# Kernel tuning notes

Measured on AMD Instinct MI355X. Metric: run time of the kernel, lower is better.

Reference implementation:

```python
import jax, jax.numpy as jnp
import numpy as np
import math

D_INNER = 512
D_STATE = 16
DT_RANK = 32
B_SZ = 2
L_SEQ = 4096


def setup_inputs() -> dict:
    key = jax.random.key(0)
    ks = jax.random.split(key, 6)
    x = jax.random.normal(ks[0], (B_SZ, L_SEQ, D_INNER), dtype=jnp.float32)
    # parameters (match torch init semantics closely enough for a numeric baseline)
    A = jnp.arange(1, D_STATE + 1, dtype=jnp.float32)
    A_log = jnp.broadcast_to(jnp.log(A)[None, :], (D_INNER, D_STATE)).copy()
    D_param = jnp.ones((D_INNER,), dtype=jnp.float32)
    # x_proj: Linear(d_inner -> dt_rank + 2*d_state), no bias
    W_xproj = jax.random.normal(ks[1], (DT_RANK + 2 * D_STATE, D_INNER), dtype=jnp.float32) / np.sqrt(D_INNER)
    # dt_proj: Linear(dt_rank -> d_inner) with special bias init
    W_dt = jax.random.normal(ks[2], (D_INNER, DT_RANK), dtype=jnp.float32) / np.sqrt(DT_RANK)
    dt_init = jnp.exp(jax.random.uniform(ks[3], (D_INNER,)) * (math.log(0.1) - math.log(0.001)) + math.log(0.001))
    b_dt = jnp.log(jnp.exp(dt_init) - 1.0)
    alpha = jnp.asarray(0.6, dtype=jnp.float32)
    beta_logit = jnp.asarray(math.log(0.99 / (1.0 - 0.99 + 1e-08)), dtype=jnp.float32)
    return {"x": x, "A_log": A_log, "D_param": D_param, "W_xproj": W_xproj,
            "W_dt": W_dt, "b_dt": b_dt, "alpha": alpha, "beta_logit": beta_logit}


def _momentum_ssm(x, A_log, D_param, W_xproj, W_dt, b_dt, alpha, beta_logit):
    # x: (B, L, D)
    proj = jnp.einsum('bld,pd->blp', x, W_xproj)            # (B, L, r+2N)
    dt_in = proj[..., :DT_RANK]
    Bp = proj[..., DT_RANK:DT_RANK + D_STATE]                # (B, L, N)
    Cp = proj[..., DT_RANK + D_STATE:]                       # (B, L, N)
    dt = jax.nn.softplus(jnp.einsum('blr,dr->bld', dt_in, W_dt) + b_dt)  # (B, L, D)
    A = -jnp.exp(A_log)                                      # (D, N)
    A_bar = jnp.exp(dt[..., None] * A[None, None])           # (B, L, D, N)
    # fused B_bar * x_t: dt * Bp * x
    inp = dt[..., None] * Bp[:, :, None, :] * x[..., None]   # (B, L, D, N)
    beta = jax.nn.sigmoid(beta_logit)

    # scan over time; carry (h, v): (B, D, N)
    h0 = jnp.zeros((x.shape[0], D_INNER, D_STATE), dtype=x.dtype)
    v0 = jnp.zeros_like(h0)

    def step(carry, ts):
        h, v = carry
        a_t, inp_t, c_t = ts                                 # (B,D,N), (B,D,N), (B,N)
        v = beta * v + alpha * inp_t
        h = a_t * h + v
        y = jnp.einsum('bdn,bn->bd', h, c_t)
        return (h, v), y

    xs = (jnp.moveaxis(A_bar, 1, 0), jnp.moveaxis(inp, 1, 0), jnp.moveaxis(Cp, 1, 0))
    _, ys = jax.lax.scan(step, (h0, v0), xs)                 # ys: (L, B, D)
    y = jnp.moveaxis(ys, 0, 1)                               # (B, L, D)
    return y + D_param * x


def reference(x, A_log, D_param, W_xproj, W_dt, b_dt, alpha, beta_logit):
    return _momentum_ssm(x, A_log, D_param, W_xproj, W_dt, b_dt, alpha, beta_logit)
```

## Files before the change

kernel.cpp:

```cpp
#include <hip/hip_runtime.h>


#define D_IN 512
#define D_ST 16
#define DTR  32
#define BSZ  2
#define LSEQ 4096
#define PDIM 64
#define NCH  256
#define LCH  (LSEQ / NCH)
#define LOG2E 1.44269504f
#define LN2   0.69314718f

typedef __attribute__((ext_vector_type(8))) short short8;
typedef __attribute__((ext_vector_type(4))) float f32x4;
typedef _Float16 f16;
typedef __attribute__((ext_vector_type(8))) _Float16 f16x8;

__device__ inline float fast_exp2(float x) { return __builtin_amdgcn_exp2f(x); }
__device__ inline float fast_log2(float x) { return __builtin_amdgcn_logf(x); }

__device__ inline unsigned short bf16_rne(float f) {
  unsigned b = __float_as_uint(f);
  return (unsigned short)((b + 0x7fffu + ((b >> 16) & 1u)) >> 16);
}

__device__ inline void cvt8(const float4 u, const float4 v, short8& hi, short8& lo) {
  float f[8] = {u.x, u.y, u.z, u.w, v.x, v.y, v.z, v.w};
#pragma unroll
  for (int i = 0; i < 8; ++i) {
    unsigned short h = bf16_rne(f[i]);
    hi[i] = (short)h;
    float r = f[i] - __uint_as_float((unsigned)h << 16);
    lo[i] = (short)bf16_rne(r);
  }
}

__device__ inline void st16h(f16* p, const float* s) {
  f16 t[16];
#pragma unroll
  for (int i = 0; i < 16; ++i) t[i] = (f16)s[i];
  *(f16x8*)p = *(f16x8*)&t[0];
  *(f16x8*)(p + 8) = *(f16x8*)&t[8];
}
__device__ inline void ld16h(const f16* p, float* d) {
  f16x8 a = *(const f16x8*)p;
  f16x8 b = *(const f16x8*)(p + 8);
#pragma unroll
  for (int i = 0; i < 8; ++i) { d[i] = (float)a[i]; d[8 + i] = (float)b[i]; }
}

#define PWCHK(val, n)                                                        \
  pw = pw && (fabsf((val) - (float)((n) + 1) * a0) <=                        \
              2e-5f * fabsf((float)((n) + 1) * a0));

__device__ inline bool detectA2(const float* __restrict__ A_log, int d, float& a0) {
  const float4* ap = (const float4*)(A_log + (size_t)d * D_ST);
  float4 r0 = ap[0], r1 = ap[1], r2 = ap[2], r3 = ap[3];
  float4 e0 = make_float4(-__expf(r0.x) * LOG2E, -__expf(r0.y) * LOG2E,
                          -__expf(r0.z) * LOG2E, -__expf(r0.w) * LOG2E);
  float4 e1 = make_float4(-__expf(r1.x) * LOG2E, -__expf(r1.y) * LOG2E,
                          -__expf(r1.z) * LOG2E, -__expf(r1.w) * LOG2E);
  float4 e2 = make_float4(-__expf(r2.x) * LOG2E, -__expf(r2.y) * LOG2E,
                          -__expf(r2.z) * LOG2E, -__expf(r2.w) * LOG2E);
  float4 e3 = make_float4(-__expf(r3.x) * LOG2E, -__expf(r3.y) * LOG2E,
                          -__expf(r3.z) * LOG2E, -__expf(r3.w) * LOG2E);
  a0 = e0.x;
  bool pw = true;
  PWCHK(e0.y, 1) PWCHK(e0.z, 2) PWCHK(e0.w, 3)
  PWCHK(e1.x, 4) PWCHK(e1.y, 5) PWCHK(e1.z, 6) PWCHK(e1.w, 7)
  PWCHK(e2.x, 8) PWCHK(e2.y, 9) PWCHK(e2.z, 10) PWCHK(e2.w, 11)
  PWCHK(e3.x, 12) PWCHK(e3.y, 13) PWCHK(e3.z, 14) PWCHK(e3.w, 15)
  return pw;
}

__global__ __launch_bounds__(256) void k_wprep(const float* __restrict__ W,
                                               short* __restrict__ Whi,
                                               short* __restrict__ Wlo) {
  const int i = (blockIdx.x * 256 + threadIdx.x) * 4;
  float4 w = *(const float4*)(W + i);
  float f[4] = {w.x, w.y, w.z, w.w};
  unsigned short h[4], lo[4];
#pragma unroll
  for (int j = 0; j < 4; ++j) {
    h[j] = bf16_rne(f[j]);
    float r = f[j] - __uint_as_float((unsigned)h[j] << 16);
    lo[j] = bf16_rne(r);
  }
  *(uint2*)(Whi + i) = make_uint2(h[0] | ((unsigned)h[1] << 16), h[2] | ((unsigned)h[3] << 16));
  *(uint2*)(Wlo + i) = make_uint2(lo[0] | ((unsigned)lo[1] << 16), lo[2] | ((unsigned)lo[3] << 16));
}

#define MM3(ACC, AH, AL, BH, BL)                                        \
  ACC = __builtin_amdgcn_mfma_f32_16x16x32_bf16(AL, BH, ACC, 0, 0, 0);  \
  ACC = __builtin_amdgcn_mfma_f32_16x16x32_bf16(AH, BL, ACC, 0, 0, 0);  \
  ACC = __builtin_amdgcn_mfma_f32_16x16x32_bf16(AH, BH, ACC, 0, 0, 0);

#define LOADB(P, S)                                   \
  {                                                   \
    const int kb = ((S) & 15) * 32;                   \
    P##h0 = *(const short8*)(bh + kb);                \
    P##h1 = *(const short8*)(bh + 8192 + kb);         \
    P##h2 = *(const short8*)(bh + 16384 + kb);        \
    P##h3 = *(const short8*)(bh + 24576 + kb);        \
    P##l0 = *(const short8*)(bl + kb);                \
    P##l1 = *(const short8*)(bl + 8192 + kb);         \
    P##l2 = *(const short8*)(bl + 16384 + kb);        \
    P##l3 = *(const short8*)(bl + 24576 + kb);        \
  }

#define LOADA(Aa, Ab, S)                              \
  {                                                   \
    const int ka = ((S) & 15) * 32;                   \
    Aa = *(const float4*)(xr + ka);                   \
    Ab = *(const float4*)(xr + ka + 4);               \
  }

#define SUBSTEP(Aa, Ab, P, SA, SB)                    \
  {                                                   \
    short8 ahi, alo;                                  \
    cvt8(Aa, Ab, ahi, alo);                           \
    MM3(acc0, ahi, alo, P##h0, P##l0);                \
    MM3(acc1, ahi, alo, P##h1, P##l1);                \
    MM3(acc2, ahi, alo, P##h2, P##l2);                \
    MM3(acc3, ahi, alo, P##h3, P##l3);                \
    LOADB(P, SB);                                     \
    LOADA(Aa, Ab, SA);                                \
  }

__global__ __launch_bounds__(64) void k_proj(const float* __restrict__ x,
                                             const short* __restrict__ Whi,
                                             const short* __restrict__ Wlo,
                                             float* __restrict__ proj) {
  const int row0 = blockIdx.x * 16;
  const int l = threadIdx.x;
  const int m = l & 15;
  const int ko = (l >> 4) * 8;
  const float* xr = x + (size_t)(row0 + m) * D_IN + ko;
  const short* bh = Whi + (size_t)m * D_IN + ko;
  const short* bl = Wlo + (size_t)m * D_IN + ko;

  f32x4 acc0 = {0.f, 0.f, 0.f, 0.f}, acc1 = acc0, acc2 = acc0, acc3 = acc0;
  float4 A0a, A0b, A1a, A1b, A2a, A2b, A3a, A3b;
  short8 Xh0, Xh1, Xh2, Xh3, Xl0, Xl1, Xl2, Xl3;
  short8 Yh0, Yh1, Yh2, Yh3, Yl0, Yl1, Yl2, Yl3;
  LOADA(A0a, A0b, 0); LOADA(A1a, A1b, 1); LOADA(A2a, A2b, 2); LOADA(A3a, A3b, 3);
  LOADB(X, 0); LOADB(Y, 1);

#pragma unroll
  for (int it = 0; it < 4; ++it) {
    const int s = it * 4;
    SUBSTEP(A0a, A0b, X, s + 4, s + 2);
    SUBSTEP(A1a, A1b, Y, s + 5, s + 3);
    SUBSTEP(A2a, A2b, X, s + 6, s + 4);
    SUBSTEP(A3a, A3b, Y, s + 7, s + 5);
  }

  const int r0 = (l >> 4) * 4;
#pragma unroll
  for (int r = 0; r < 4; ++r) {
    float* pr = proj + (size_t)(row0 + r0 + r) * PDIM + m;
    pr[0] = acc0[r]; pr[16] = acc1[r]; pr[32] = acc2[r]; pr[48] = acc3[r];
  }
}

#define S1_LOOP                                                              \
  _Pragma("unroll")                                                          \
  for (int j = 0; j < LCH; ++j) {                                            \
    const float4* pj = (const float4*)(pb + j * PDIM);                       \
    float4 pp[8];                                                            \
    _Pragma("unroll")                                                        \
    for (int k = 0; k < 8; ++k) pp[k] = pj[k];                               \
    float c0 = bb, c1 = 0.f, c2 = 0.f, c3 = 0.f;                             \
    _Pragma("unroll")                                                        \
    for (int k = 0; k < 8; ++k) {                                            \
      c0 = fmaf(pp[k].x, w4[k].x, c0);                                       \
      c1 = fmaf(pp[k].y, w4[k].y, c1);                                       \
      c2 = fmaf(pp[k].z, w4[k].z, c2);                                       \
      c3 = fmaf(pp[k].w, w4[k].w, c3);                                       \
    }                                                                        \
    const float acc = (c0 + c1) + (c2 + c3);                                 \
    const float ee = fast_exp2(acc * LOG2E);                                 \
    const float dtc = (acc > 20.f) ? acc : LN2 * fast_log2(1.f + ee);        \
    dp[(size_t)j * D_IN] = (f16)dtc;                                         \
    sd += dtc;                                                               \
    bpow *= beta;                                                            \
    const float u = alpha * dtc * xs[j];                                     \
    float4 bq[4];                                                            \
    _Pragma("unroll")                                                        \
    for (int k = 0; k < 4; ++k) bq[k] = pj[8 + k];                           \
    const float* Bf = (const float*)bq;                                      \
    AR_INIT;                                                                 \
    _Pragma("unroll")                                                        \
    for (int n = 0; n < 16; ++n) {                                           \
      AR_STEP;                                                               \
      v[n] = fmaf(beta, v[n], u * Bf[n]);                                    \
      h[n] = fmaf(ar, h[n], v[n]);                                           \
      cv[n] = fmaf(ar, cv[n], bpow);                                         \
    }                                                                        \
  }

__global__ __launch_bounds__(256) void k_scan1(const float* __restrict__ x,
                                               const float* __restrict__ proj,
                                               const float* __restrict__ A_log,
                                               const float* __restrict__ W_dt,
                                               const float* __restrict__ b_dt,
                                               const float* __restrict__ alpha_p,
                                               const float* __restrict__ beta_p,
                                               f16* __restrict__ hh,
                                               f16* __restrict__ vh,
                                               f16* __restrict__ cvv,
                                               float* __restrict__ sdt,
                                               f16* __restrict__ dth) {
  const int c = blockIdx.x, b = blockIdx.z;
  const int d = blockIdx.y * 256 + threadIdx.x;
  const int t0 = c * LCH;
  const float* pb = proj + ((size_t)b * LSEQ + t0) * PDIM;

  float xs[LCH];
  {
    const float* xp = x + ((size_t)b * LSEQ + t0) * D_IN + d;
#pragma unroll
    for (int j = 0; j < LCH; ++j) xs[j] = xp[(size_t)j * D_IN];
  }
  float4 w4[8];
  {
    const float4* wp = (const float4*)(W_dt + (size_t)d * DTR);
#pragma unroll
    for (int i = 0; i < 8; ++i) w4[i] = wp[i];
  }
  const float bb = b_dt[d];
  const float alpha = alpha_p[0];
  const float beta = 1.f / (1.f + __expf(-beta_p[0]));
  float a0;
  const bool pw = detectA2(A_log, d, a0);

  f16* dp = dth + ((size_t)b * LSEQ + t0) * D_IN + d;
  float h[16] = {}, v[16] = {}, cv[16] = {};
  float bpow = 1.f, sd = 0.f;

  if (pw) {
#define AR_INIT const float r = fast_exp2(dtc * a0); float ar = 1.f
#define AR_STEP ar *= r
    S1_LOOP
#undef AR_INIT
#undef AR_STEP
  } else {
    volatile const float* av = A_log + (size_t)d * D_ST;
#define AR_INIT float ar
#define AR_STEP ar = fast_exp2(dtc * (-__expf(av[n]) * LOG2E))
    S1_LOOP
#undef AR_INIT
#undef AR_STEP
  }

  const size_t base = ((size_t)(b * NCH + c) * D_IN + d) * D_ST;
  st16h(hh + base, h);
  st16h(vh + base, v);
  st16h(cvv + base, cv);
  sdt[(size_t)(b * NCH + c) * D_IN + d] = sd;
}

__global__ __launch_bounds__(64) void k_fix(f16* __restrict__ hh,
                                            f16* __restrict__ vh,
                                            const f16* __restrict__ cvv,
                                            const float* __restrict__ sdt,
                                            const float* __restrict__ A_log,
                                            const float* __restrict__ beta_p) {
  const int g = blockIdx.x * 64 + threadIdx.x;
  const int b = g >> 13;
  const int dn = g & 8191;
  const float beta = 1.f / (1.f + __expf(-beta_p[0]));
  const float A2 = -__expf(A_log[dn]) * LOG2E;
  float bL = beta;
#pragma unroll
  for (int i = 0; i < 4; ++i) bL *= bL;

  const size_t cs = (size_t)D_IN * D_ST;
  const size_t base = (size_t)b * NCH * cs + dn;
  const size_t sbase = (size_t)b * NCH * D_IN + (dn >> 4);

  float hg[8], vg[8], cg[8], sg[8];
#pragma unroll
  for (int i = 0; i < 8; ++i) {
    hg[i] = (float)hh[base + i * cs];
    vg[i] = (float)vh[base + i * cs];
    cg[i] = (float)cvv[base + i * cs];
    sg[i] = sdt[sbase + i * D_IN];
  }
  float H = 0.f, V = 0.f;
  for (int c0 = 0; c0 < NCH; c0 += 8) {
    const int cp = (c0 + 8) & (NCH - 1);
    float hn[8], vn[8], cn[8], sn[8];
#pragma unroll
    for (int i = 0; i < 8; ++i) {
      hn[i] = (float)hh[base + (size_t)(cp + i) * cs];
      vn[i] = (float)vh[base + (size_t)(cp + i) * cs];
      cn[i] = (float)cvv[base + (size_t)(cp + i) * cs];
      sn[i] = sdt[sbase + (size_t)(cp + i) * D_IN];
    }
#pragma unroll
    for (int i = 0; i < 8; ++i) {
      hh[base + (size_t)(c0 + i) * cs] = (f16)H;
      vh[base + (size_t)(c0 + i) * cs] = (f16)V;
      const float Pa = fast_exp2(sg[i] * A2);
      const float Hn = fmaf(Pa, H, fmaf(cg[i], V, hg[i]));
      V = fmaf(bL, V, vg[i]);
      H = Hn;
    }
#pragma unroll
    for (int i = 0; i < 8; ++i) { hg[i] = hn[i]; vg[i] = vn[i]; cg[i] = cn[i]; sg[i] = sn[i]; }
  }
}

#define S2_LOOP                                                              \
  _Pragma("unroll")                                                          \
  for (int j = 0; j < LCH; ++j) {                                            \
    const float4* pj = (const float4*)(pb + j * PDIM);                       \
    float4 bq[8];                                                            \
    _Pragma("unroll")                                                        \
    for (int k = 0; k < 8; ++k) bq[k] = pj[8 + k];                           \
    const float* Bf = (const float*)bq;                                      \
    const float dtc = dtv[j], xv = xs[j];                                    \
    const float u = alpha * dtc * xv;                                        \
    float y0 = 0.f, y1 = 0.f, y2 = 0.f, y3 = 0.f;                            \
    AR_INIT;                                                                 \
    _Pragma("unroll")                                                        \
    for (int n = 0; n < 16; ++n) {                                           \
      AR_STEP;                                                               \
      v[n] = fmaf(beta, v[n], u * Bf[n]);                                    \
      h[n] = fmaf(ar, h[n], v[n]);                                           \
      float hc = h[n] * Bf[16 + n];                                          \
      if ((n & 3) == 0) y0 += hc;                                            \
      else if ((n & 3) == 1) y1 += hc;                                       \
      else if ((n & 3) == 2) y2 += hc;                                       \
      else y3 += hc;                                                         \
    }                                                                        \
    op[(size_t)j * D_IN] = (y0 + y1) + (y2 + y3) + Dv * xv;                  \
  }

__global__ __launch_bounds__(256) void k_scan2(const float* __restrict__ x,
                                               const f16* __restrict__ dth,
                                               const float* __restrict__ proj,
                                               const float* __restrict__ A_log,
                                               const float* __restrict__ D_param,
                                               const float* __restrict__ alpha_p,
                                               const float* __restrict__ beta_p,
                                               const f16* __restrict__ hh,
                                               const f16* __restrict__ vh,
                                               float* __restrict__ out) {
  const int c = blockIdx.x, b = blockIdx.z;
  const int d = blockIdx.y * 256 + threadIdx.x;
  const int t0 = c * LCH;
  const float* pb = proj + ((size_t)b * LSEQ + t0) * PDIM;

  float xs[LCH], dtv[LCH];
  {
    const float* xp = x + ((size_t)b * LSEQ + t0) * D_IN + d;
    const f16* dp = dth + ((size_t)b * LSEQ + t0) * D_IN + d;
#pragma unroll
    for (int j = 0; j < LCH; ++j) xs[j] = xp[(size_t)j * D_IN];
#pragma unroll
    for (int j = 0; j < LCH; ++j) dtv[j] = (float)dp[(size_t)j * D_IN];
  }
  const float alpha = alpha_p[0];
  const float beta = 1.f / (1.f + __expf(-beta_p[0]));
  const float Dv = D_param[d];
  float a0;
  const bool pw = detectA2(A_log, d, a0);
  const size_t ibase = ((size_t)(b * NCH + c) * D_IN + d) * D_ST;
  float h[16], v[16];
  ld16h(hh + ibase, h);
  ld16h(vh + ibase, v);

  float* op = out + ((size_t)b * LSEQ + t0) * D_IN + d;
  if (pw) {
#define AR_INIT const float r = fast_exp2(dtc * a0); float ar = 1.f
#define AR_STEP ar *= r
    S2_LOOP
#undef AR_INIT
#undef AR_STEP
  } else {
    volatile const float* av = A_log + (size_t)d * D_ST;
#define AR_INIT float ar
#define AR_STEP ar = fast_exp2(dtc * (-__expf(av[n]) * LOG2E))
    S2_LOOP
#undef AR_INIT
#undef AR_STEP
  }
}

extern "C" void kernel_launch(void* const* d_in, const int* in_sizes, int n_in,
                              void* d_out, int out_size, void* d_ws, size_t ws_size,
                              hipStream_t stream) {
  const float* x = (const float*)d_in[0];
  const float* A_log = (const float*)d_in[1];
  const float* D_param = (const float*)d_in[2];
  const float* W_xproj = (const float*)d_in[3];
  const float* W_dt = (const float*)d_in[4];
  const float* b_dt = (const float*)d_in[5];
  const float* alpha = (const float*)d_in[6];
  const float* beta_logit = (const float*)d_in[7];
  float* out = (float*)d_out;

  const size_t NST = (size_t)BSZ * NCH * D_IN * D_ST;
  float* ws = (float*)d_ws;
  float* proj = ws;
  float* sdt = proj + (size_t)BSZ * LSEQ * PDIM;
  f16* hh = (f16*)(sdt + (size_t)BSZ * NCH * D_IN);
  f16* vh = hh + NST;
  f16* cvv = vh + NST;
  f16* dth = cvv + NST;
  short* Whi = (short*)(dth + (size_t)BSZ * LSEQ * D_IN);
  short* Wlo = Whi + (size_t)PDIM * D_IN;

  k_wprep<<<dim3(PDIM * D_IN / 1024), dim3(256), 0, stream>>>(W_xproj, Whi, Wlo);
  k_proj<<<dim3(BSZ * LSEQ / 16), dim3(64), 0, stream>>>(x, Whi, Wlo, proj);
  k_scan1<<<dim3(NCH, D_IN / 256, BSZ), dim3(256), 0, stream>>>(
      x, proj, A_log, W_dt, b_dt, alpha, beta_logit, hh, vh, cvv, sdt, dth);
  k_fix<<<dim3(BSZ * D_IN * D_ST / 64), dim3(64), 0, stream>>>(hh, vh, cvv, sdt, A_log,
                                                               beta_logit);
  k_scan2<<<dim3(NCH, D_IN / 256, BSZ), dim3(256), 0, stream>>>(
      x, dth, proj, A_log, D_param, alpha, beta_logit, hh, vh, out);
}
```

Measured before the change: 175.9 us.

## Split projection K across four waves with LDS reduction; deepen fix prefetch

The projection kernel now uses 256 threads per 16-row block. Each of four waves handles a 128-wide slice of the K dimension, and the partial accumulators are summed through shared memory before a vectorized store. This gives more parallelism per block and shortens each wave's serial MFMA chain, at the cost of an LDS round trip and a barrier. Separately, the chunk-fix kernel prefetches 16 chunks at a time instead of 8, which hides more load latency but uses more registers.

```diff
diff --git a/kernel.cpp b/kernel.cpp
--- a/kernel.cpp
+++ b/kernel.cpp
@@ -98,7 +98,7 @@
 
 #define LOADB(P, S)                                   \
   {                                                   \
-    const int kb = ((S) & 15) * 32;                   \
+    const int kb = (S) * 32;                          \
     P##h0 = *(const short8*)(bh + kb);                \
     P##h1 = *(const short8*)(bh + 8192 + kb);         \
     P##h2 = *(const short8*)(bh + 16384 + kb);        \
@@ -111,12 +111,12 @@
 
 #define LOADA(Aa, Ab, S)                              \
   {                                                   \
-    const int ka = ((S) & 15) * 32;                   \
+    const int ka = (S) * 32;                          \
     Aa = *(const float4*)(xr + ka);                   \
     Ab = *(const float4*)(xr + ka + 4);               \
   }
 
-#define SUBSTEP(Aa, Ab, P, SA, SB)                    \
+#define COMPSTEP(Aa, Ab, P)                           \
   {                                                   \
     short8 ahi, alo;                                  \
     cvt8(Aa, Ab, ahi, alo);                           \
@@ -124,18 +124,18 @@
     MM3(acc1, ahi, alo, P##h1, P##l1);                \
     MM3(acc2, ahi, alo, P##h2, P##l2);                \
     MM3(acc3, ahi, alo, P##h3, P##l3);                \
-    LOADB(P, SB);                                     \
-    LOADA(Aa, Ab, SA);                                \
-  }
-
-__global__ __launch_bounds__(64) void k_proj(const float* __restrict__ x,
-                                             const short* __restrict__ Whi,
-                                             const short* __restrict__ Wlo,
-                                             float* __restrict__ proj) {
+  }
+
+__global__ __launch_bounds__(256) void k_proj(const float* __restrict__ x,
+                                              const short* __restrict__ Whi,
+                                              const short* __restrict__ Wlo,
+                                              float* __restrict__ proj) {
+  __shared__ float Pacc[4][16][64];
   const int row0 = blockIdx.x * 16;
-  const int l = threadIdx.x;
+  const int l = threadIdx.x & 63;
+  const int wq = threadIdx.x >> 6;
   const int m = l & 15;
-  const int ko = (l >> 4) * 8;
+  const int ko = (l >> 4) * 8 + wq * 128;
   const float* xr = x + (size_t)(row0 + m) * D_IN + ko;
   const short* bh = Whi + (size_t)m * D_IN + ko;
   const short* bl = Wlo + (size_t)m * D_IN + ko;
@@ -147,21 +147,30 @@
   LOADA(A0a, A0b, 0); LOADA(A1a, A1b, 1); LOADA(A2a, A2b, 2); LOADA(A3a, A3b, 3);
   LOADB(X, 0); LOADB(Y, 1);
 
-#pragma unroll
-  for (int it = 0; it < 4; ++it) {
-    const int s = it * 4;
-    SUBSTEP(A0a, A0b, X, s + 4, s + 2);
-    SUBSTEP(A1a, A1b, Y, s + 5, s + 3);
-    SUBSTEP(A2a, A2b, X, s + 6, s + 4);
-    SUBSTEP(A3a, A3b, Y, s + 7, s + 5);
-  }
+  COMPSTEP(A0a, A0b, X); LOADB(X, 2);
+  COMPSTEP(A1a, A1b, Y); LOADB(Y, 3);
+  COMPSTEP(A2a, A2b, X);
+  COMPSTEP(A3a, A3b, Y);
 
   const int r0 = (l >> 4) * 4;
 #pragma unroll
   for (int r = 0; r < 4; ++r) {
-    float* pr = proj + (size_t)(row0 + r0 + r) * PDIM + m;
-    pr[0] = acc0[r]; pr[16] = acc1[r]; pr[32] = acc2[r]; pr[48] = acc3[r];
-  }
+    Pacc[wq][r0 + r][m] = acc0[r];
+    Pacc[wq][r0 + r][16 + m] = acc1[r];
+    Pacc[wq][r0 + r][32 + m] = acc2[r];
+    Pacc[wq][r0 + r][48 + m] = acc3[r];
+  }
+  __syncthreads();
+
+  const int orow = threadIdx.x >> 4;
+  const int ocol = (threadIdx.x & 15) * 4;
+  float4 s0 = *(const float4*)&Pacc[0][orow][ocol];
+  float4 s1 = *(const float4*)&Pacc[1][orow][ocol];
+  float4 s2 = *(const float4*)&Pacc[2][orow][ocol];
+  float4 s3 = *(const float4*)&Pacc[3][orow][ocol];
+  float4 o = make_float4((s0.x + s1.x) + (s2.x + s3.x), (s0.y + s1.y) + (s2.y + s3.y),
+                         (s0.z + s1.z) + (s2.z + s3.z), (s0.w + s1.w) + (s2.w + s3.w));
+  *(float4*)(proj + (size_t)(row0 + orow) * PDIM + ocol) = o;
 }
 
 #define S1_LOOP                                                              \
@@ -280,27 +289,27 @@
   const size_t base = (size_t)b * NCH * cs + dn;
   const size_t sbase = (size_t)b * NCH * D_IN + (dn >> 4);
 
-  float hg[8], vg[8], cg[8], sg[8];
-#pragma unroll
-  for (int i = 0; i < 8; ++i) {
+  float hg[16], vg[16], cg[16], sg[16];
+#pragma unroll
+  for (int i = 0; i < 16; ++i) {
     hg[i] = (float)hh[base + i * cs];
     vg[i] = (float)vh[base + i * cs];
     cg[i] = (float)cvv[base + i * cs];
     sg[i] = sdt[sbase + i * D_IN];
   }
   float H = 0.f, V = 0.f;
-  for (int c0 = 0; c0 < NCH; c0 += 8) {
-    const int cp = (c0 + 8) & (NCH - 1);
-    float hn[8], vn[8], cn[8], sn[8];
-#pragma unroll
-    for (int i = 0; i < 8; ++i) {
+  for (int c0 = 0; c0 < NCH; c0 += 16) {
+    const int cp = (c0 + 16) & (NCH - 1);
+    float hn[16], vn[16], cn[16], sn[16];
+#pragma unroll
+    for (int i = 0; i < 16; ++i) {
       hn[i] = (float)hh[base + (size_t)(cp + i) * cs];
       vn[i] = (float)vh[base + (size_t)(cp + i) * cs];
       cn[i] = (float)cvv[base + (size_t)(cp + i) * cs];
       sn[i] = sdt[sbase + (size_t)(cp + i) * D_IN];
     }
 #pragma unroll
-    for (int i = 0; i < 8; ++i) {
+    for (int i = 0; i < 16; ++i) {
       hh[base + (size_t)(c0 + i) * cs] = (f16)H;
       vh[base + (size_t)(c0 + i) * cs] = (f16)V;
       const float Pa = fast_exp2(sg[i] * A2);
@@ -309,7 +318,7 @@
       H = Hn;
     }
 #pragma unroll
-    for (int i = 0; i < 8; ++i) { hg[i] = hn[i]; vg[i] = vn[i]; cg[i] = cn[i]; sg[i] = sn[i]; }
+    for (int i = 0; i < 16; ++i) { hg[i] = hn[i]; vg[i] = vn[i]; cg[i] = cn[i]; sg[i] = sn[i]; }
   }
 }
 
@@ -415,7 +424,7 @@
   short* Wlo = Whi + (size_t)PDIM * D_IN;
 
   k_wprep<<<dim3(PDIM * D_IN / 1024), dim3(256), 0, stream>>>(W_xproj, Whi, Wlo);
-  k_proj<<<dim3(BSZ * LSEQ / 16), dim3(64), 0, stream>>>(x, Whi, Wlo, proj);
+  k_proj<<<dim3(BSZ * LSEQ / 16), dim3(256), 0, stream>>>(x, Whi, Wlo, proj);
   k_scan1<<<dim3(NCH, D_IN / 256, BSZ), dim3(256), 0, stream>>>(
       x, proj, A_log, W_dt, b_dt, alpha, beta_logit, hh, vh, cvv, sdt, dth);
   k_fix<<<dim3(BSZ * D_IN * D_ST / 64), dim3(64), 0, stream>>>(hh, vh, cvv, sdt, A_log,
```

New measurement: 167.8 us. -4.6%, faster.
